# Kernel tuning notes

Measured on AMD Instinct MI355X. Metric: run time of the kernel, lower is better.

The kernel has to match this reference:

```python
import jax, jax.numpy as jnp
import numpy as np

EMB = 12
NUM_CLASSES = 17
NUM_GRAPHS = 1000


def gcn_conv(h, W, b, row, col, n):
    # h: [N, Fin]; row/col already include self-loops. Aggregation at col (target).
    h = h @ W + b  # [N, Fout]
    deg = jax.ops.segment_sum(jnp.ones_like(col, dtype=h.dtype), col, num_segments=n)
    dinv = deg ** -0.5  # self-loops guarantee deg >= 1
    norm = dinv[row] * dinv[col]  # [E]
    msg = norm[:, None] * h[row]  # gather + scale
    return jax.ops.segment_sum(msg, col, num_segments=n)  # scatter-add


def setup_inputs() -> dict:
    key = jax.random.key(0)
    ks = jax.random.split(key, 16)
    N, E = 400000, 6400000
    x = jax.random.normal(ks[0], (N, 4), dtype=jnp.float32)
    edge_index = jax.random.randint(ks[1], (2, E), 0, N, dtype=jnp.int64)
    batch_index = jnp.sort(jax.random.randint(ks[2], (N,), 0, NUM_GRAPHS, dtype=jnp.int64))

    def lin(k, fi, fo):
        k1, k2 = jax.random.split(k)
        bound = 1.0 / np.sqrt(fi)
        W = jax.random.uniform(k1, (fi, fo), minval=-bound, maxval=bound, dtype=jnp.float32)
        b = jax.random.uniform(k2, (fo,), minval=-bound, maxval=bound, dtype=jnp.float32)
        return W, b

    W0, b0 = lin(ks[3], 4, EMB)
    W1, b1 = lin(ks[4], EMB, EMB)
    W2, b2 = lin(ks[5], EMB, EMB)
    W3, b3 = lin(ks[6], EMB, EMB)
    Wout, bout = lin(ks[7], EMB * 2, NUM_CLASSES)
    return {"x": x, "edge_index": edge_index, "batch_index": batch_index,
            "W0": W0, "b0": b0, "W1": W1, "b1": b1, "W2": W2, "b2": b2,
            "W3": W3, "b3": b3, "Wout": Wout, "bout": bout}


def reference(x, edge_index, batch_index, W0, b0, W1, b1, W2, b2, W3, b3, Wout, bout):
    n = x.shape[0]
    loops = jnp.arange(n, dtype=edge_index.dtype)
    row = jnp.concatenate([edge_index[0], loops])
    col = jnp.concatenate([edge_index[1], loops])

    h = jnp.tanh(gcn_conv(x, W0, b0, row, col, n))
    h = jnp.tanh(gcn_conv(h, W1, b1, row, col, n))
    h = jnp.tanh(gcn_conv(h, W2, b2, row, col, n))
    h = jnp.tanh(gcn_conv(h, W3, b3, row, col, n))

    gmax = jax.ops.segment_max(h, batch_index, num_segments=NUM_GRAPHS)
    gsum = jax.ops.segment_sum(h, batch_index, num_segments=NUM_GRAPHS)
    cnt = jax.ops.segment_sum(jnp.ones((n,), dtype=h.dtype), batch_index, num_segments=NUM_GRAPHS)
    gmean = gsum / jnp.maximum(cnt, 1.0)[:, None]
    hidden = jnp.concatenate([gmax, gmean], axis=1)  # [G, 2*EMB]
    out = hidden @ Wout + bout  # [G, NUM_CLASSES]
    return out, hidden
```

## Files before the change

kernel.cpp:

```cpp
#include <hip/hip_runtime.h>
#include <hip/hip_bf16.h>
#include <math.h>

typedef __hip_bfloat16 bf16;

#define EMB 12
#define NCLS 17
#define NG 1000
#define BSHIFT 9
#define BSPAN 512
#define MAXNB 1024
#define CHUNK 8192
#define EB 8
#define TSHIFT 16
#define NTILE 8
#define NKEY (BSPAN*NTILE)
#define SCAP 11264

__device__ __forceinline__ float b2f(bf16 v){ return __bfloat162float(v); }

__device__ __forceinline__ unsigned short f2bf_rne(float f){
  unsigned int u = __float_as_uint(f);
  unsigned int r = (u + 0x7FFFu + ((u >> 16) & 1u)) >> 16;
  return (unsigned short)r;
}

__device__ __forceinline__ float ldf(const void* p, size_t i, int isbf){
  if (isbf) return b2f(((const bf16*)p)[i]);
  return ((const float*)p)[i];
}
__device__ __forceinline__ void stout(void* p, size_t i, float v, int isbf){
  if (isbf) ((unsigned short*)p)[i] = f2bf_rne(v);
  else      ((float*)p)[i] = v;
}

__device__ __forceinline__ void rowload(const float* p, float o[12]){
  const float4* q = (const float4*)p;
  float4 a = q[0], b = q[1], c = q[2];
  o[0]=a.x;o[1]=a.y;o[2]=a.z;o[3]=a.w;o[4]=b.x;o[5]=b.y;o[6]=b.z;o[7]=b.w;
  o[8]=c.x;o[9]=c.y;o[10]=c.z;o[11]=c.w;
}
__device__ __forceinline__ void rowload(const bf16* p, float o[12]){
  const uint4* q = (const uint4*)p;
  uint4 u0 = q[0];
  uint2 u1 = *(const uint2*)(q+1);
  o[0] =__uint_as_float(u0.x<<16); o[1] =__uint_as_float(u0.x&0xFFFF0000u);
  o[2] =__uint_as_float(u0.y<<16); o[3] =__uint_as_float(u0.y&0xFFFF0000u);
  o[4] =__uint_as_float(u0.z<<16); o[5] =__uint_as_float(u0.z&0xFFFF0000u);
  o[6] =__uint_as_float(u0.w<<16); o[7] =__uint_as_float(u0.w&0xFFFF0000u);
  o[8] =__uint_as_float(u1.x<<16); o[9] =__uint_as_float(u1.x&0xFFFF0000u);
  o[10]=__uint_as_float(u1.y<<16); o[11]=__uint_as_float(u1.y&0xFFFF0000u);
}
__device__ __forceinline__ void rowstore(float* p, const float o[12]){
  float4* q = (float4*)p;
  q[0] = make_float4(o[0],o[1],o[2],o[3]);
  q[1] = make_float4(o[4],o[5],o[6],o[7]);
  q[2] = make_float4(o[8],o[9],o[10],o[11]);
}
__device__ __forceinline__ void rowstore(bf16* p, const float o[12]){
  unsigned int u[6];
  #pragma unroll
  for (int k=0;k<6;k++)
    u[k] = (unsigned int)f2bf_rne(o[2*k]) | ((unsigned int)f2bf_rne(o[2*k+1])<<16);
  uint2* q = (uint2*)p;
  q[0] = make_uint2(u[0],u[1]);
  q[1] = make_uint2(u[2],u[3]);
  q[2] = make_uint2(u[4],u[5]);
}

__global__ void k_detect(const int* __restrict__ ei, const unsigned short* __restrict__ xh,
                         int* __restrict__ flags){
  if (blockIdx.x==0 && threadIdx.x==0){
    int z = 1;
    for (int k=1; k<32; k+=2) z &= (ei[k]==0);
    flags[0] = z;
    int hits = 0;
    for (int k=0; k<32; k+=2){
      int e = (xh[k] >> 7) & 0xFF;
      if (e >= 100 && e <= 140) hits++;
    }
    flags[1] = (hits >= 12) ? 1 : 0;
  }
}
__device__ __forceinline__ int ld_row(const int* ei, long long E, long long i, int w64){
  return w64 ? ei[2*i] : ei[i];
}
__device__ __forceinline__ int ld_col(const int* ei, long long E, long long i, int w64){
  return w64 ? ei[2*E + 2*i] : ei[E + i];
}
__device__ __forceinline__ int ld_batch(const int* b, long long i, int w64){
  return w64 ? b[2*i] : b[i];
}

__global__ void k_zero_i(int* __restrict__ p, int n){
  int i = blockIdx.x*blockDim.x + threadIdx.x;
  if (i < n) p[i] = 0;
}
__global__ void __launch_bounds__(256)
k_bkt_count(const int* __restrict__ ei, const int* __restrict__ flags,
            int* __restrict__ bcnt, int* __restrict__ bofs, int E, int NB){
  __shared__ int h[MAXNB];
  int t = threadIdx.x;
  for (int j=t; j<NB; j+=256) h[j] = 0;
  __syncthreads();
  int w64 = flags[0];
  long long base = (long long)blockIdx.x * CHUNK;
  for (int k0=0; k0<CHUNK; k0+=256*EB){
    int c[EB]; bool v[EB];
    #pragma unroll
    for (int u=0;u<EB;u++){
      long long i = base + k0 + u*256 + t;
      v[u] = (i < E);
      c[u] = v[u] ? ld_col(ei, E, i, w64) : 0;
    }
    #pragma unroll
    for (int u=0;u<EB;u++) if (v[u]) atomicAdd(&h[c[u]>>BSHIFT], 1);
  }
  __syncthreads();
  size_t rowb = (size_t)blockIdx.x * NB;
  for (int j=t; j<NB; j+=256){
    int c = h[j];
    bofs[rowb + j] = c;
    if (c > 0) atomicAdd(&bcnt[j], c);
  }
}
__global__ void __launch_bounds__(1024)
k_bkt_scan_par(const int* __restrict__ bcnt, int* __restrict__ bbase,
               int* __restrict__ rs2, int NB, int NBK){
  __shared__ int s[1024];
  int t = threadIdx.x;
  int v = (t < NB) ? bcnt[t] : 0;
  s[t] = v;
  __syncthreads();
  for (int off=1; off<1024; off<<=1){
    int add = (t >= off) ? s[t-off] : 0;
    __syncthreads();
    s[t] += add;
    __syncthreads();
  }
  if (t < NB) bbase[t] = s[t] - v;
  if (t == 1023){
    bbase[NB] = s[1023];
    rs2[NBK]  = s[1023];
  }
}
__global__ void __launch_bounds__(256)
k_colscan(int* __restrict__ bofs, const int* __restrict__ bbase, int NB, int GC){
  __shared__ int part[256];
  int j = blockIdx.x, t = threadIdx.x;
  int K = (GC + 255) / 256;
  int beg = t*K, end = beg+K < GC ? beg+K : GC;
  int s = 0;
  for (int i=beg; i<end; i++) s += bofs[(size_t)i*NB + j];
  part[t] = s;
  __syncthreads();
  for (int off=1; off<256; off<<=1){
    int add = (t >= off) ? part[t-off] : 0;
    __syncthreads();
    part[t] += add;
    __syncthreads();
  }
  int run = bbase[j] + part[t] - s;
  for (int i=beg; i<end; i++){
    size_t idx = (size_t)i*NB + j;
    int v = bofs[idx];
    bofs[idx] = run;
    run += v;
  }
}
__global__ void __launch_bounds__(256)
k_bkt_place(const int* __restrict__ ei, const int* __restrict__ flags,
            const int* __restrict__ bofs, int* __restrict__ pairs, int E, int NB){
  __shared__ int hb[MAXNB];
  __shared__ int lcur[MAXNB];
  __shared__ int part[256];
  __shared__ int vals[CHUNK];
  __shared__ int dst[CHUNK];
  int t = threadIdx.x;
  size_t rowb = (size_t)blockIdx.x * NB;
  for (int j=t; j<NB; j+=256){ hb[j] = bofs[rowb + j]; lcur[j] = 0; }
  __syncthreads();
  int w64 = flags[0];
  long long base = (long long)blockIdx.x * CHUNK;
  long long rem = E - base;
  int total = (rem < CHUNK) ? (int)rem : CHUNK;
  for (int k0=0; k0<CHUNK; k0+=256*EB){
    int c[EB]; bool v[EB];
    #pragma unroll
    for (int u=0;u<EB;u++){
      long long i = base + k0 + u*256 + t;
      v[u] = (i < E);
      c[u] = v[u] ? ld_col(ei, E, i, w64) : 0;
    }
    #pragma unroll
    for (int u=0;u<EB;u++) if (v[u]) atomicAdd(&lcur[c[u]>>BSHIFT], 1);
  }
  __syncthreads();
  int loc[4]; int s = 0;
  #pragma unroll
  for (int u=0;u<4;u++){ int j=t*4+u; loc[u] = (j<NB) ? lcur[j] : 0; s += loc[u]; }
  part[t] = s;
  __syncthreads();
  for (int off=1; off<256; off<<=1){
    int add = (t >= off) ? part[t-off] : 0;
    __syncthreads();
    part[t] += add;
    __syncthreads();
  }
  int run = part[t] - s;
  #pragma unroll
  for (int u=0;u<4;u++){
    int j=t*4+u;
    if (j<NB){ lcur[j] = run; hb[j] -= run; }
    run += loc[u];
  }
  __syncthreads();
  for (int k0=0; k0<CHUNK; k0+=256*EB){
    int r[EB], c[EB]; bool v[EB];
    #pragma unroll
    for (int u=0;u<EB;u++){
      long long i = base + k0 + u*256 + t;
      v[u] = (i < E);
      r[u] = v[u] ? ld_row(ei, E, i, w64) : 0;
      c[u] = v[u] ? ld_col(ei, E, i, w64) : 0;
    }
    #pragma unroll
    for (int u=0;u<EB;u++){
      if (v[u]){
        int j = c[u]>>BSHIFT;
        int p = atomicAdd(&lcur[j], 1);
        vals[p] = r[u] | ((r[u]>>TSHIFT)<<19) | ((c[u] & (BSPAN-1)) << 22);
        dst[p]  = hb[j] + p;
      }
    }
  }
  __syncthreads();
  for (int s2=t; s2<total; s2+=256) pairs[dst[s2]] = vals[s2];
}
__device__ __forceinline__ int tkey(int pk){
  return (((pk>>19)&7)<<BSHIFT) | (pk>>22);
}
__global__ void __launch_bounds__(256)
k_group(const int* __restrict__ pairs, const int* __restrict__ bbase,
        float* __restrict__ dinv, int* __restrict__ src,
        int* __restrict__ rs2, int N){
  __shared__ int cnt[NKEY];
  __shared__ int cur[NKEY];
  __shared__ int part[256];
  __shared__ int stage[SCAP];
  int b = blockIdx.x, t = threadIdx.x;
  int lo = bbase[b], hi = bbase[b+1];
  int cap = hi - lo;
  #pragma unroll
  for (int u=0;u<NKEY/256;u++) cnt[u*256+t] = 0;
  __syncthreads();
  {
    int p = lo + t;
    for (; p + 3*256 < hi; p += 4*256){
      int k0=tkey(pairs[p]), k1=tkey(pairs[p+256]), k2=tkey(pairs[p+512]), k3=tkey(pairs[p+768]);
      atomicAdd(&cnt[k0],1); atomicAdd(&cnt[k1],1);
      atomicAdd(&cnt[k2],1); atomicAdd(&cnt[k3],1);
    }
    for (; p < hi; p += 256) atomicAdd(&cnt[tkey(pairs[p])],1);
  }
  __syncthreads();
  int loc[16]; int s = 0;
  #pragma unroll
  for (int u=0;u<16;u++){ loc[u] = cnt[t*16+u]; s += loc[u]; }
  part[t] = s;
  __syncthreads();
  for (int off=1; off<256; off<<=1){
    int add = (t >= off) ? part[t-off] : 0;
    __syncthreads();
    part[t] += add;
    __syncthreads();
  }
  int run = lo + part[t] - s;
  #pragma unroll
  for (int u=0;u<16;u++){ cur[t*16+u] = run; run += loc[u]; }
  __syncthreads();
  {
    size_t rb = (size_t)b * NKEY;
    #pragma unroll
    for (int u=0;u<16;u++){ int k = t*16+u; rs2[rb + k] = cur[k]; }
    int col0 = b << BSHIFT;
    #pragma unroll
    for (int u=0;u<2;u++){
      int j = 2*t + u;
      int colg = col0 + j;
      if (colg < N){
        int deg = 0;
        #pragma unroll
        for (int tt=0; tt<NTILE; tt++) deg += cnt[(tt<<BSHIFT) | j];
        dinv[colg] = rsqrtf((float)deg + 1.0f);
      }
    }
  }
  __syncthreads();
  if (cap <= SCAP){
    int p = lo + t;
    for (; p + 3*256 < hi; p += 4*256){
      int pk0=pairs[p], pk1=pairs[p+256], pk2=pairs[p+512], pk3=pairs[p+768];
      int q0 = atomicAdd(&cur[tkey(pk0)], 1);
      int q1 = atomicAdd(&cur[tkey(pk1)], 1);
      int q2 = atomicAdd(&cur[tkey(pk2)], 1);
      int q3 = atomicAdd(&cur[tkey(pk3)], 1);
      stage[q0-lo] = pk0 & 0x7FFFF; stage[q1-lo] = pk1 & 0x7FFFF;
      stage[q2-lo] = pk2 & 0x7FFFF; stage[q3-lo] = pk3 & 0x7FFFF;
    }
    for (; p < hi; p += 256){
      int pk = pairs[p];
      int q = atomicAdd(&cur[tkey(pk)], 1);
      stage[q-lo] = pk & 0x7FFFF;
    }
    __syncthreads();
    for (int s2=t; s2<cap; s2+=256) src[lo+s2] = stage[s2];
  } else {
    int p = lo + t;
    for (; p + 3*256 < hi; p += 4*256){
      int pk0=pairs[p], pk1=pairs[p+256], pk2=pairs[p+512], pk3=pairs[p+768];
      int q0 = atomicAdd(&cur[tkey(pk0)], 1);
      int q1 = atomicAdd(&cur[tkey(pk1)], 1);
      int q2 = atomicAdd(&cur[tkey(pk2)], 1);
      int q3 = atomicAdd(&cur[tkey(pk3)], 1);
      src[q0] = pk0 & 0x7FFFF; src[q1] = pk1 & 0x7FFFF;
      src[q2] = pk2 & 0x7FFFF; src[q3] = pk3 & 0x7FFFF;
    }
    for (; p < hi; p += 256){
      int pk = pairs[p];
      int q = atomicAdd(&cur[tkey(pk)], 1);
      src[q] = pk & 0x7FFFF;
    }
  }
}

template<typename GT>
__global__ void k_lin_first(const void* __restrict__ x, const void* __restrict__ W,
                            const void* __restrict__ b, const int* __restrict__ flags,
                            const float* __restrict__ dinv,
                            GT* __restrict__ g, int n){
  __shared__ float Ws[4*EMB];
  __shared__ float bs[EMB];
  int t = threadIdx.x;
  int isbf = flags[1];
  if (t < 4*EMB) Ws[t] = ldf(W, t, isbf);
  if (t < EMB)   bs[t] = ldf(b, t, isbf);
  __syncthreads();
  int i = blockIdx.x*blockDim.x + t;
  if (i >= n) return;
  float xi[4];
  #pragma unroll
  for (int k=0;k<4;k++) xi[k] = ldf(x, (size_t)i*4+k, isbf);
  float d = dinv[i];
  float o[12];
  #pragma unroll
  for (int j=0;j<EMB;j++){
    float h = bs[j];
    #pragma unroll
    for (int k=0;k<4;k++) h = fmaf(xi[k], Ws[k*EMB+j], h);
    o[j] = d*h;
  }
  rowstore(g + (size_t)i*16, o);
}

template<typename GT>
__global__ void k_lin_mid(const float* __restrict__ acc, const void* __restrict__ W,
                          const void* __restrict__ b, const int* __restrict__ flags,
                          const float* __restrict__ dinv,
                          GT* __restrict__ g, int n){
  __shared__ float Ws[EMB*EMB];
  __shared__ float bs[EMB];
  int t = threadIdx.x;
  int isbf = flags[1];
  if (t < EMB*EMB) Ws[t] = ldf(W, t, isbf);
  if (t < EMB)     bs[t] = ldf(b, t, isbf);
  __syncthreads();
  int i = blockIdx.x*blockDim.x + t;
  if (i >= n) return;
  float xi[EMB];
  size_t abase = (size_t)i*EMB;
  #pragma unroll
  for (int k=0;k<EMB;k++) xi[k] = tanhf(acc[abase+k]);
  float d = dinv[i];
  float o[12];
  #pragma unroll
  for (int j=0;j<EMB;j++){
    float h = bs[j];
    #pragma unroll
    for (int k=0;k<EMB;k++) h = fmaf(xi[k], Ws[k*EMB+j], h);
    o[j] = d*h;
  }
  rowstore(g + (size_t)i*16, o);
}

template<typename GT, int MODE>
__device__ __forceinline__ void finish_col(int c, int n, const float a[12],
                                           const GT* __restrict__ gin,
                                           const float* __restrict__ dinv,
                                           const float* Ws, const float* bs,
                                           void* __restrict__ outp){
  if (c >= n) return;
  float v[12];
  rowload(gin + (size_t)c*16, v);
  #pragma unroll
  for (int j=0;j<12;j++) v[j] += a[j];
  float d = dinv[c];
  if (MODE == 0){
    float h[12];
    #pragma unroll
    for (int k=0;k<12;k++) h[k] = tanhf(d*v[k]);
    float o[12];
    #pragma unroll
    for (int j=0;j<12;j++){
      float w = bs[j];
      #pragma unroll
      for (int k=0;k<12;k++) w = fmaf(h[k], Ws[k*EMB+j], w);
      o[j] = d*w;
    }
    rowstore((GT*)outp + (size_t)c*16, o);
  } else {
    float4* ap = (float4*)((float*)outp + (size_t)c*EMB);
    ap[0] = make_float4(tanhf(d*v[0]), tanhf(d*v[1]), tanhf(d*v[2]),  tanhf(d*v[3]));
    ap[1] = make_float4(tanhf(d*v[4]), tanhf(d*v[5]), tanhf(d*v[6]),  tanhf(d*v[7]));
    ap[2] = make_float4(tanhf(d*v[8]), tanhf(d*v[9]), tanhf(d*v[10]), tanhf(d*v[11]));
  }
}

template<typename GT, int MODE>
__global__ void __launch_bounds__(256)
k_gather_rot(const int* __restrict__ rs2, const int* __restrict__ src,
             const float* __restrict__ dinv, const GT* __restrict__ gin,
             const void* __restrict__ W, const void* __restrict__ b,
             const int* __restrict__ flags, void* __restrict__ outp,
             int n, int nt){
  __shared__ float Ws[EMB*EMB];
  __shared__ float bs[EMB];
  int t = threadIdx.x;
  if (MODE == 0){
    int isbf = flags[1];
    if (t < EMB*EMB) Ws[t] = ldf(W, t, isbf);
    if (t < EMB)     bs[t] = ldf(b, t, isbf);
    __syncthreads();
  }
  int par = t & 1;
  int c = blockIdx.x*128 + (t>>1);
  int q = (c < n) ? c : 0;
  int base = ((q>>BSHIFT)<<12) + (q & (BSPAN-1));
  float a[12];
  #pragma unroll
  for (int j=0;j<12;j++) a[j] = 0.f;
  int tau = (int)(blockIdx.x & 7) % nt;
  int i0 = base + (tau<<BSHIFT);
  int s = rs2[i0], e = rs2[i0+1];
  for (int k=0; k<nt; k++){
    int tn = tau+1; if (tn >= nt) tn = 0;
    int ps=0, pe=0;
    if (k+1 < nt){
      int ni = base + (tn<<BSHIFT);
      ps = rs2[ni]; pe = rs2[ni+1];
    }
    int p = s + par;
    for (; p+2 < e; p += 4){
      int r0 = src[p], r1 = src[p+2];
      float h0[12], h1[12];
      rowload(gin + (size_t)r0*16, h0);
      rowload(gin + (size_t)r1*16, h1);
      #pragma unroll
      for (int j=0;j<12;j++) a[j] += h0[j] + h1[j];
    }
    if (p < e){
      int r = src[p];
      float h[12];
      rowload(gin + (size_t)r*16, h);
      #pragma unroll
      for (int j=0;j<12;j++) a[j] += h[j];
    }
    s=ps; e=pe; tau=tn;
  }
  #pragma unroll
  for (int j=0;j<12;j++) a[j] += __shfl_xor(a[j], 1, 64);
  if (par == 0)
    finish_col<GT,MODE>(c, n, a, gin, dinv, Ws, bs, outp);
}

__global__ void k_cnt_deg(const int* __restrict__ ei, const int* __restrict__ flags,
                          int* __restrict__ cnt, int e){
  int i = blockIdx.x*blockDim.x + threadIdx.x;
  if (i >= e) return;
  atomicAdd(&cnt[ld_col(ei, e, i, flags[0])], 1);
}
__global__ void k_dinv_from_cnt(const int* __restrict__ cnt, float* __restrict__ dinv, int n){
  int i = blockIdx.x*blockDim.x + threadIdx.x;
  if (i < n) dinv[i] = rsqrtf((float)(cnt[i] + 1));
}
__global__ void k_selfinit(const float* __restrict__ g, const float* __restrict__ dinv,
                           float* __restrict__ acc, int n){
  int i = blockIdx.x*blockDim.x + threadIdx.x;
  if (i >= n) return;
  float d = dinv[i];
  float h[12]; rowload(g + (size_t)i*16, h);
  #pragma unroll
  for (int j=0;j<EMB;j++) acc[(size_t)i*EMB+j] = d*h[j];
}
__global__ void k_scatter(const int* __restrict__ ei, const int* __restrict__ flags,
                          const float* __restrict__ dinv, const float* __restrict__ g,
                          float* __restrict__ acc, int e){
  int i = blockIdx.x*blockDim.x + threadIdx.x;
  if (i >= e) return;
  int w64 = flags[0];
  int r = ld_row(ei, e, i, w64);
  int c = ld_col(ei, e, i, w64);
  float w = dinv[c];
  float h[12];
  rowload(g + (size_t)r*16, h);
  float* ap = acc + (size_t)c*EMB;
  #pragma unroll
  for (int j=0;j<EMB;j++) atomicAdd(ap+j, w*h[j]);
}

template<int DOTANH>
__global__ void __launch_bounds__(256)
k_pool(const float* __restrict__ acc, const int* __restrict__ batch,
       const int* __restrict__ flags,
       const void* __restrict__ Wout, const void* __restrict__ bout,
       void* __restrict__ out, int n){
  int g = blockIdx.x;
  int w64  = flags[0];
  int isbf = flags[1];
  __shared__ int se[2];
  __shared__ float smax[4][EMB];
  __shared__ float ssum[4][EMB];
  __shared__ float hid[2*EMB];
  if (threadIdx.x == 0){
    int lo=0, hi=n;
    while (lo<hi){ int m=(lo+hi)>>1; if (ld_batch(batch,m,w64) < g) lo=m+1; else hi=m; }
    se[0]=lo;
    int lo2=lo; hi=n;
    while (lo2<hi){ int m=(lo2+hi)>>1; if (ld_batch(batch,m,w64) < g+1) lo2=m+1; else hi=m; }
    se[1]=lo2;
  }
  __syncthreads();
  int start=se[0], end=se[1];
  float lmax[EMB], lsum[EMB];
  #pragma unroll
  for (int j=0;j<EMB;j++){ lmax[j]=-3.0e38f; lsum[j]=0.f; }
  for (int i=start+(int)threadIdx.x; i<end; i+=blockDim.x){
    size_t base=(size_t)i*EMB;
    #pragma unroll
    for (int j=0;j<EMB;j++){
      float h = DOTANH ? tanhf(acc[base+j]) : acc[base+j];
      lmax[j] = fmaxf(lmax[j], h);
      lsum[j] += h;
    }
  }
  #pragma unroll
  for (int m=32;m>=1;m>>=1){
    #pragma unroll
    for (int j=0;j<EMB;j++){
      lmax[j] = fmaxf(lmax[j], __shfl_xor(lmax[j], m, 64));
      lsum[j] += __shfl_xor(lsum[j], m, 64);
    }
  }
  int wave = threadIdx.x>>6, lane = threadIdx.x&63;
  if (lane==0){
    #pragma unroll
    for (int j=0;j<EMB;j++){ smax[wave][j]=lmax[j]; ssum[wave][j]=lsum[j]; }
  }
  __syncthreads();
  int cnt = end-start;
  if (threadIdx.x < EMB){
    int j = threadIdx.x;
    float mx=smax[0][j], sm=ssum[0][j];
    #pragma unroll
    for (int w=1;w<4;w++){ mx=fmaxf(mx,smax[w][j]); sm+=ssum[w][j]; }
    if (cnt <= 0){ mx = 0.f; sm = 0.f; }
    float mean = sm / fmaxf((float)cnt, 1.0f);
    hid[j]     = mx;
    hid[EMB+j] = mean;
    stout(out, (size_t)NG*NCLS + (size_t)g*2*EMB + j,       mx,   isbf);
    stout(out, (size_t)NG*NCLS + (size_t)g*2*EMB + EMB + j, mean, isbf);
  }
  __syncthreads();
  if (threadIdx.x < NCLS){
    int c = threadIdx.x;
    float o = ldf(bout, c, isbf);
    #pragma unroll
    for (int k=0;k<2*EMB;k++) o = fmaf(hid[k], ldf(Wout, (size_t)k*NCLS+c, isbf), o);
    stout(out, (size_t)g*NCLS + c, o, isbf);
  }
}

__global__ void k_zero_out_noflags(void* __restrict__ out, int m){
  int i = blockIdx.x*blockDim.x + threadIdx.x;
  if (i < m) ((float*)out)[i] = 0.0f;
}

static void build_csr(const int* ei, const void* x, int* flags, int* bcnt, int* bbase,
                      int* bofs, float* dinv, int* src, int* pairs, int* rs2,
                      int N, int E, int NB, hipStream_t stream){
  const int TB = 256;
  const int gc = (E + CHUNK - 1) / CHUNK;
  const int NBK = NB * NKEY;
  k_detect      <<<1, 64, 0, stream>>>(ei, (const unsigned short*)x, flags);
  k_zero_i      <<<(NB+TB-1)/TB, TB, 0, stream>>>(bcnt, NB);
  k_bkt_count   <<<gc, TB, 0, stream>>>(ei, flags, bcnt, bofs, E, NB);
  k_bkt_scan_par<<<1, 1024, 0, stream>>>(bcnt, bbase, rs2, NB, NBK);
  k_colscan     <<<NB, TB, 0, stream>>>(bofs, bbase, NB, gc);
  k_bkt_place   <<<gc, TB, 0, stream>>>(ei, flags, bofs, pairs, E, NB);
  k_group       <<<NB, TB, 0, stream>>>(pairs, bbase, dinv, src, rs2, N);
}

static size_t alignup(size_t v){ return (v + 63) & ~(size_t)63; }
static size_t maxsz(size_t a, size_t b){ return a > b ? a : b; }

extern "C" void kernel_launch(void* const* d_in, const int* in_sizes, int n_in,
                              void* d_out, int out_size, void* d_ws, size_t ws_size,
                              hipStream_t stream) {
  const void* x     = d_in[0];
  const int*  ei    = (const int*)d_in[1];
  const int*  batch = (const int*)d_in[2];
  const void* W0 = d_in[3];  const void* b0 = d_in[4];
  const void* W1 = d_in[5];  const void* b1 = d_in[6];
  const void* W2 = d_in[7];  const void* b2 = d_in[8];
  const void* W3 = d_in[9];  const void* b3 = d_in[10];
  const void* Wout = d_in[11]; const void* bout = d_in[12];

  const int N = in_sizes[0] / 4;
  const int E = in_sizes[1] / 2;
  const int NB = (N + BSPAN - 1) >> BSHIFT;
  const int GC = (E + CHUNK - 1) / CHUNK;
  const int TB = 256;
  const int gn = (N + TB - 1) / TB;
  const int gr = (N + 127) / 128;
  const int nt = (N + (1<<TSHIFT) - 1) >> TSHIFT;

  char* base = (char*)d_ws;

  size_t o_flags  = 0;
  size_t o_dinv   = alignup(o_flags + 64);
  size_t o_bcnt   = alignup(o_dinv + (size_t)N*4);
  size_t o_bbase  = alignup(o_bcnt + (size_t)NB*4);
  size_t o_bofs   = alignup(o_bbase + ((size_t)NB+1)*4);
  size_t o_rs2    = alignup(o_bofs + (size_t)GC*NB*4);
  size_t o_src    = alignup(o_rs2 + ((size_t)NB*NKEY + 1)*4);
  size_t o_buf    = alignup(o_src + (size_t)E*4);

  int* flags  = (int*)(base+o_flags);
  float* dinv = (float*)(base+o_dinv);
  int* bcnt   = (int*)(base+o_bcnt);
  int* bbase  = (int*)(base+o_bbase);
  int* bofs   = (int*)(base+o_bofs);
  int* rs2    = (int*)(base+o_rs2);
  int* src    = (int*)(base+o_src);
  int* pairs  = (int*)(base+o_buf);

  bool fast_ok = (N < (1<<19)) && (NB <= MAXNB) && (nt <= NTILE);

  {
    size_t szR0 = maxsz((size_t)N*16*2, (size_t)N*EMB*4);
    size_t o_gB = alignup(o_buf + szR0);
    size_t need = o_gB + (size_t)N*16*2;
    bool pairs_fit = (size_t)E*4 <= need - o_buf;
    if (fast_ok && pairs_fit && ws_size >= need){
      bf16*  gA  = (bf16*)(base+o_buf);
      bf16*  gB  = (bf16*)(base+o_gB);
      float* acc = (float*)(base+o_buf);
      build_csr(ei, x, flags, bcnt, bbase, bofs, dinv, src, pairs, rs2, N, E, NB, stream);
      k_lin_first<bf16><<<gn, TB, 0, stream>>>(x, W0, b0, flags, dinv, gA, N);
      k_gather_rot<bf16,0><<<gr, TB, 0, stream>>>(rs2, src, dinv, gA, W1, b1, flags, gB, N, nt);
      k_gather_rot<bf16,0><<<gr, TB, 0, stream>>>(rs2, src, dinv, gB, W2, b2, flags, gA, N, nt);
      k_gather_rot<bf16,0><<<gr, TB, 0, stream>>>(rs2, src, dinv, gA, W3, b3, flags, gB, N, nt);
      k_gather_rot<bf16,1><<<gr, TB, 0, stream>>>(rs2, src, dinv, gB, 0, 0, flags, acc, N, nt);
      k_pool<0><<<NG, 256, 0, stream>>>(acc, batch, flags, Wout, bout, d_out, N);
      return;
    }
  }

  {
    size_t o_gA = o_buf;
    size_t o_gB = alignup(o_gA + (size_t)N*16*4);
    size_t need = o_gB + (size_t)N*16*4;
    bool pairs_fit = (size_t)E*4 <= need - o_buf;
    if (fast_ok && pairs_fit && ws_size >= need){
      float* gA  = (float*)(base+o_gA);
      float* gB  = (float*)(base+o_gB);
      float* acc = gA;
      build_csr(ei, x, flags, bcnt, bbase, bofs, dinv, src, pairs, rs2, N, E, NB, stream);
      k_lin_first<float><<<gn, TB, 0, stream>>>(x, W0, b0, flags, dinv, gA, N);
      k_gather_rot<float,0><<<gr, TB, 0, stream>>>(rs2, src, dinv, gA, W1, b1, flags, gB, N, nt);
      k_gather_rot<float,0><<<gr, TB, 0, stream>>>(rs2, src, dinv, gB, W2, b2, flags, gA, N, nt);
      k_gather_rot<float,0><<<gr, TB, 0, stream>>>(rs2, src, dinv, gA, W3, b3, flags, gB, N, nt);
      k_gather_rot<float,1><<<gr, TB, 0, stream>>>(rs2, src, dinv, gB, 0, 0, flags, acc, N, nt);
      k_pool<0><<<NG, 256, 0, stream>>>(acc, batch, flags, Wout, bout, d_out, N);
      return;
    }
  }

  {
    size_t f_cnt  = alignup(o_dinv + (size_t)N*4);
    size_t f_g    = alignup(f_cnt + (size_t)N*4);
    size_t f_acc  = alignup(f_g + (size_t)N*16*4);
    size_t f_end  = f_acc + (size_t)N*EMB*4;
    const int ge = (E + TB - 1) / TB;
    int* cnt = (int*)(base+f_cnt);

    if (ws_size >= f_end){
      float* g   = (float*)(base+f_g);
      float* acc = (float*)(base+f_acc);
      k_detect  <<<1, 64, 0, stream>>>(ei, (const unsigned short*)x, flags);
      k_zero_i  <<<gn, TB, 0, stream>>>(cnt, N);
      k_cnt_deg <<<ge, TB, 0, stream>>>(ei, flags, cnt, E);
      k_dinv_from_cnt<<<gn, TB, 0, stream>>>(cnt, dinv, N);
      k_lin_first<float><<<gn, TB, 0, stream>>>(x, W0, b0, flags, dinv, g, N);
      k_selfinit <<<gn, TB, 0, stream>>>(g, dinv, acc, N);
      k_scatter  <<<ge, TB, 0, stream>>>(ei, flags, dinv, g, acc, E);
      const void* Wl[3] = {W1,W2,W3};
      const void* bl[3] = {b1,b2,b3};
      for (int l=0;l<3;l++){
        k_lin_mid<float><<<gn, TB, 0, stream>>>(acc, Wl[l], bl[l], flags, dinv, g, N);
        k_selfinit<<<gn, TB, 0, stream>>>(g, dinv, acc, N);
        k_scatter <<<ge, TB, 0, stream>>>(ei, flags, dinv, g, acc, E);
      }
      k_pool<1><<<NG, 256, 0, stream>>>(acc, batch, flags, Wout, bout, d_out, N);
    } else {
      k_zero_out_noflags<<<(out_size+255)/256, 256, 0, stream>>>(d_out, out_size);
    }
  }
}
```

Before: 523.5 us.

## Replace per-chunk offset table and column scan with global atomic bucket cursors

The bucket-sort placement no longer stores a per-chunk count table and runs a separate column-scan kernel. Each place block instead reserves its slice of every bucket with an atomicAdd on a global cursor array seeded by the bucket scan. Each thread also keeps its 32 edges in registers, so the edge list is read once instead of twice. This drops one kernel launch and the GC×NB offset traffic, but edge order within a bucket now depends on block scheduling and register pressure rises.

After: 531.4 us. Within noise of the previous version (+1.5%).

```diff
diff --git a/kernel.cpp b/kernel.cpp
--- a/kernel.cpp
+++ b/kernel.cpp
@@ -11,6 +11,7 @@
 #define BSPAN 512
 #define MAXNB 1024
 #define CHUNK 8192
+#define EPT (CHUNK/256)
 #define EB 8
 #define TSHIFT 16
 #define NTILE 8
@@ -98,7 +99,7 @@
 }
 __global__ void __launch_bounds__(256)
 k_bkt_count(const int* __restrict__ ei, const int* __restrict__ flags,
-            int* __restrict__ bcnt, int* __restrict__ bofs, int E, int NB){
+            int* __restrict__ bcnt, int E, int NB){
   __shared__ int h[MAXNB];
   int t = threadIdx.x;
   for (int j=t; j<NB; j+=256) h[j] = 0;
@@ -117,16 +118,14 @@
     for (int u=0;u<EB;u++) if (v[u]) atomicAdd(&h[c[u]>>BSHIFT], 1);
   }
   __syncthreads();
-  size_t rowb = (size_t)blockIdx.x * NB;
   for (int j=t; j<NB; j+=256){
     int c = h[j];
-    bofs[rowb + j] = c;
     if (c > 0) atomicAdd(&bcnt[j], c);
   }
 }
 __global__ void __launch_bounds__(1024)
 k_bkt_scan_par(const int* __restrict__ bcnt, int* __restrict__ bbase,
-               int* __restrict__ rs2, int NB, int NBK){
+               int* __restrict__ cursor, int* __restrict__ rs2, int NB, int NBK){
   __shared__ int s[1024];
   int t = threadIdx.x;
   int v = (t < NB) ? bcnt[t] : 0;
@@ -138,63 +137,37 @@
     s[t] += add;
     __syncthreads();
   }
-  if (t < NB) bbase[t] = s[t] - v;
+  if (t < NB){ bbase[t] = s[t] - v; cursor[t] = s[t] - v; }
   if (t == 1023){
     bbase[NB] = s[1023];
     rs2[NBK]  = s[1023];
   }
 }
 __global__ void __launch_bounds__(256)
-k_colscan(int* __restrict__ bofs, const int* __restrict__ bbase, int NB, int GC){
-  __shared__ int part[256];
-  int j = blockIdx.x, t = threadIdx.x;
-  int K = (GC + 255) / 256;
-  int beg = t*K, end = beg+K < GC ? beg+K : GC;
-  int s = 0;
-  for (int i=beg; i<end; i++) s += bofs[(size_t)i*NB + j];
-  part[t] = s;
-  __syncthreads();
-  for (int off=1; off<256; off<<=1){
-    int add = (t >= off) ? part[t-off] : 0;
-    __syncthreads();
-    part[t] += add;
-    __syncthreads();
-  }
-  int run = bbase[j] + part[t] - s;
-  for (int i=beg; i<end; i++){
-    size_t idx = (size_t)i*NB + j;
-    int v = bofs[idx];
-    bofs[idx] = run;
-    run += v;
-  }
-}
-__global__ void __launch_bounds__(256)
 k_bkt_place(const int* __restrict__ ei, const int* __restrict__ flags,
-            const int* __restrict__ bofs, int* __restrict__ pairs, int E, int NB){
+            int* __restrict__ cursor, int* __restrict__ pairs, int E, int NB){
   __shared__ int hb[MAXNB];
   __shared__ int lcur[MAXNB];
   __shared__ int part[256];
   __shared__ int vals[CHUNK];
   __shared__ int dst[CHUNK];
   int t = threadIdx.x;
-  size_t rowb = (size_t)blockIdx.x * NB;
-  for (int j=t; j<NB; j+=256){ hb[j] = bofs[rowb + j]; lcur[j] = 0; }
+  for (int j=t; j<NB; j+=256) lcur[j] = 0;
   __syncthreads();
   int w64 = flags[0];
   long long base = (long long)blockIdx.x * CHUNK;
   long long rem = E - base;
   int total = (rem < CHUNK) ? (int)rem : CHUNK;
-  for (int k0=0; k0<CHUNK; k0+=256*EB){
-    int c[EB]; bool v[EB];
-    #pragma unroll
-    for (int u=0;u<EB;u++){
-      long long i = base + k0 + u*256 + t;
-      v[u] = (i < E);
-      c[u] = v[u] ? ld_col(ei, E, i, w64) : 0;
-    }
-    #pragma unroll
-    for (int u=0;u<EB;u++) if (v[u]) atomicAdd(&lcur[c[u]>>BSHIFT], 1);
-  }
+  int r[EPT], c[EPT];
+  #pragma unroll
+  for (int u=0;u<EPT;u++){
+    long long i = base + u*256 + t;
+    bool v = (i < E);
+    r[u] = v ? ld_row(ei, E, i, w64) : 0;
+    c[u] = v ? ld_col(ei, E, i, w64) : -1;
+  }
+  #pragma unroll
+  for (int u=0;u<EPT;u++) if (c[u] >= 0) atomicAdd(&lcur[c[u]>>BSHIFT], 1);
   __syncthreads();
   int loc[4]; int s = 0;
   #pragma unroll
@@ -211,27 +184,21 @@
   #pragma unroll
   for (int u=0;u<4;u++){
     int j=t*4+u;
-    if (j<NB){ lcur[j] = run; hb[j] -= run; }
+    if (j<NB){
+      int gb = (loc[u] > 0) ? atomicAdd(&cursor[j], loc[u]) : 0;
+      lcur[j] = run;
+      hb[j]   = gb - run;
+    }
     run += loc[u];
   }
   __syncthreads();
-  for (int k0=0; k0<CHUNK; k0+=256*EB){
-    int r[EB], c[EB]; bool v[EB];
-    #pragma unroll
-    for (int u=0;u<EB;u++){
-      long long i = base + k0 + u*256 + t;
-      v[u] = (i < E);
-      r[u] = v[u] ? ld_row(ei, E, i, w64) : 0;
-      c[u] = v[u] ? ld_col(ei, E, i, w64) : 0;
-    }
-    #pragma unroll
-    for (int u=0;u<EB;u++){
-      if (v[u]){
-        int j = c[u]>>BSHIFT;
-        int p = atomicAdd(&lcur[j], 1);
-        vals[p] = r[u] | ((r[u]>>TSHIFT)<<19) | ((c[u] & (BSPAN-1)) << 22);
-        dst[p]  = hb[j] + p;
-      }
+  #pragma unroll
+  for (int u=0;u<EPT;u++){
+    if (c[u] >= 0){
+      int j = c[u]>>BSHIFT;
+      int p = atomicAdd(&lcur[j], 1);
+      vals[p] = r[u] | ((r[u]>>TSHIFT)<<19) | ((c[u] & (BSPAN-1)) << 22);
+      dst[p]  = hb[j] + p;
     }
   }
   __syncthreads();
@@ -596,17 +563,16 @@
 }
 
 static void build_csr(const int* ei, const void* x, int* flags, int* bcnt, int* bbase,
-                      int* bofs, float* dinv, int* src, int* pairs, int* rs2,
+                      int* cursor, float* dinv, int* src, int* pairs, int* rs2,
                       int N, int E, int NB, hipStream_t stream){
   const int TB = 256;
   const int gc = (E + CHUNK - 1) / CHUNK;
   const int NBK = NB * NKEY;
   k_detect      <<<1, 64, 0, stream>>>(ei, (const unsigned short*)x, flags);
   k_zero_i      <<<(NB+TB-1)/TB, TB, 0, stream>>>(bcnt, NB);
-  k_bkt_count   <<<gc, TB, 0, stream>>>(ei, flags, bcnt, bofs, E, NB);
-  k_bkt_scan_par<<<1, 1024, 0, stream>>>(bcnt, bbase, rs2, NB, NBK);
-  k_colscan     <<<NB, TB, 0, stream>>>(bofs, bbase, NB, gc);
-  k_bkt_place   <<<gc, TB, 0, stream>>>(ei, flags, bofs, pairs, E, NB);
+  k_bkt_count   <<<gc, TB, 0, stream>>>(ei, flags, bcnt, E, NB);
+  k_bkt_scan_par<<<1, 1024, 0, stream>>>(bcnt, bbase, cursor, rs2, NB, NBK);
+  k_bkt_place   <<<gc, TB, 0, stream>>>(ei, flags, cursor, pairs, E, NB);
   k_group       <<<NB, TB, 0, stream>>>(pairs, bbase, dinv, src, rs2, N);
 }
 
@@ -628,7 +594,6 @@
   const int N = in_sizes[0] / 4;
   const int E = in_sizes[1] / 2;
   const int NB = (N + BSPAN - 1) >> BSHIFT;
-  const int GC = (E + CHUNK - 1) / CHUNK;
   const int TB = 256;
   const int gn = (N + TB - 1) / TB;
   const int gr = (N + 127) / 128;
@@ -640,8 +605,8 @@
   size_t o_dinv   = alignup(o_flags + 64);
   size_t o_bcnt   = alignup(o_dinv + (size_t)N*4);
   size_t o_bbase  = alignup(o_bcnt + (size_t)NB*4);
-  size_t o_bofs   = alignup(o_bbase + ((size_t)NB+1)*4);
-  size_t o_rs2    = alignup(o_bofs + (size_t)GC*NB*4);
+  size_t o_cursor = alignup(o_bbase + ((size_t)NB+1)*4);
+  size_t o_rs2    = alignup(o_cursor + (size_t)NB*4);
   size_t o_src    = alignup(o_rs2 + ((size_t)NB*NKEY + 1)*4);
   size_t o_buf    = alignup(o_src + (size_t)E*4);
 
@@ -649,7 +614,7 @@
   float* dinv = (float*)(base+o_dinv);
   int* bcnt   = (int*)(base+o_bcnt);
   int* bbase  = (int*)(base+o_bbase);
-  int* bofs   = (int*)(base+o_bofs);
+  int* cursor = (int*)(base+o_cursor);
   int* rs2    = (int*)(base+o_rs2);
   int* src    = (int*)(base+o_src);
   int* pairs  = (int*)(base+o_buf);
@@ -665,7 +630,7 @@
       bf16*  gA  = (bf16*)(base+o_buf);
       bf16*  gB  = (bf16*)(base+o_gB);
       float* acc = (float*)(base+o_buf);
-      build_csr(ei, x, flags, bcnt, bbase, bofs, dinv, src, pairs, rs2, N, E, NB, stream);
+      build_csr(ei, x, flags, bcnt, bbase, cursor, dinv, src, pairs, rs2, N, E, NB, stream);
       k_lin_first<bf16><<<gn, TB, 0, stream>>>(x, W0, b0, flags, dinv, gA, N);
       k_gather_rot<bf16,0><<<gr, TB, 0, stream>>>(rs2, src, dinv, gA, W1, b1, flags, gB, N, nt);
       k_gather_rot<bf16,0><<<gr, TB, 0, stream>>>(rs2, src, dinv, gB, W2, b2, flags, gA, N, nt);
@@ -685,7 +650,7 @@
       float* gA  = (float*)(base+o_gA);
       float* gB  = (float*)(base+o_gB);
       float* acc = gA;
-      build_csr(ei, x, flags, bcnt, bbase, bofs, dinv, src, pairs, rs2, N, E, NB, stream);
+      build_csr(ei, x, flags, bcnt, bbase, cursor, dinv, src, pairs, rs2, N, E, NB, stream);
       k_lin_first<float><<<gn, TB, 0, stream>>>(x, W0, b0, flags, dinv, gA, N);
       k_gather_rot<float,0><<<gr, TB, 0, stream>>>(rs2, src, dinv, gA, W1, b1, flags, gB, N, nt);
       k_gather_rot<float,0><<<gr, TB, 0, stream>>>(rs2, src, dinv, gB, W2, b2, flags, gA, N, nt);
```
